# Performance work log

Measured on AMD Instinct MI355X. Metric: run time of the kernel, lower is better.

## Reference

```python
import jax, jax.numpy as jnp
import numpy as np


def _next_pow2(n: int) -> int:
    # matches torch: 2 ** ceil(log2(n))
    return 1 << (int(n) - 1).bit_length()


def setup_inputs() -> dict:
    key = jax.random.key(0)
    k1, k2 = jax.random.split(key)
    B, T, L = 256, 32768, 32768
    x = jax.random.normal(k1, (B, T), dtype=jnp.float32)
    filt = jax.random.normal(k2, (1, L), dtype=jnp.float32)
    return {"x": x, "filt": filt}


def reference(x, filt):
    """EpochedFutureFill.forward: exact causal convolution of x with filt.

    The per-token epoched algorithm (tau-step direct sum + FutureFill FFT
    cache refresh every K steps, cache initialized to zero) computes exactly
    y[b, t] = sum_{s=0}^{min(t, L-1)} filt[0, s] * x[b, t-s].
    We compute it with one FFT-based linear convolution, mirroring the
    float32 FFT math of future_fill().
    """
    B, T = x.shape
    L = filt.shape[-1]
    n_fft = _next_pow2(T + L - 1)
    xf = jnp.fft.rfft(x.astype(jnp.float32), n=n_fft)          # (B, n_fft//2+1)
    wf = jnp.fft.rfft(filt.astype(jnp.float32), n=n_fft)       # (1, n_fft//2+1)
    y = jnp.fft.irfft(xf * wf, n=n_fft)[:, :T]                 # causal lags 0..T-1
    return y.astype(x.dtype)
```

## Files before the change

kernel.cpp:

```cpp
#include <hip/hip_runtime.h>
#include <cstdint>

typedef __attribute__((ext_vector_type(8))) short short8;
typedef __attribute__((ext_vector_type(4))) float floatx4;

#define TWO_PI 6.283185307179586f

__device__ __forceinline__ unsigned short f2bf(float f) {
  union { float f; uint32_t u; } c; c.f = f;
  uint32_t u = c.u;
  u += 0x7FFFu + ((u >> 16) & 1u);
  return (unsigned short)(u >> 16);
}
__device__ __forceinline__ uint32_t packbf(float re, float im) {
  return (uint32_t)f2bf(re) | ((uint32_t)f2bf(im) << 16);
}


__global__ __launch_bounds__(256) void prep_all(
    const float* __restrict__ x, const float* __restrict__ filt,
    unsigned short* __restrict__ A1, unsigned short* __restrict__ A2,
    unsigned short* __restrict__ A3, unsigned short* __restrict__ A4,
    uint32_t* __restrict__ Zp, float2* __restrict__ Gw,
    float2* __restrict__ Tw) {
  __shared__ float2 roots[256];
  const int bid = blockIdx.x;
  const int tid = threadIdx.x;
  const float w256 = TWO_PI / 256.0f;
  if (bid < 3072) {
    int idx = bid * 256 + tid;
    if (idx < 131072) {
      int col = idx & 255, row = idx >> 8;
      int k1 = row >> 1, d = row & 1, r = col >> 1, e = col & 1;
      float th = (float)((k1 * r) & 255) * w256;
      float sn, cs; __sincosf(th, &sn, &cs);
      A1[idx] = f2bf(d == 0 ? (e == 0 ? cs : sn) : (e == 0 ? -sn : cs));
    } else if (idx < 393216) {
      int j = idx - 131072;
      int col = j & 511, row = j >> 9;
      int k2 = row >> 1, d = row & 1, cc = col >> 1, e = col & 1;
      float th = (float)((k2 * cc) & 255) * w256;
      float sn, cs; __sincosf(th, &sn, &cs);
      A2[j] = f2bf(d == 0 ? (e == 0 ? cs : sn) : (e == 0 ? -sn : cs));
    } else if (idx < 655360) {
      int j = idx - 393216;
      int col = j & 511, row = j >> 9;
      int cc = row >> 1, d = row & 1, k2 = col >> 1, e = col & 1;
      float th = (float)((k2 * cc) & 255) * w256;
      float sn, cs; __sincosf(th, &sn, &cs);
      A3[j] = f2bf(d == 0 ? (e == 0 ? cs : -sn) : (e == 0 ? sn : cs));
    } else {
      int j = idx - 655360;
      int col = j & 511, row = j >> 9;
      int r = row >> 1, d = row & 1, k1 = col >> 1, e = col & 1;
      float th = (float)((k1 * r) & 255) * w256;
      float sn, cs; __sincosf(th, &sn, &cs);
      A4[j] = f2bf(d == 0 ? (e == 0 ? cs : -sn) : (e == 0 ? sn : cs));
    }
  } else if (bid < 4096) {
    int b2 = bid - 3072;
    int s = b2 >> 3, rq = b2 & 7;
    const float* x0 = x + (size_t)(2 * s) * 32768;
    const float* x1 = x0 + 32768;
    uint32_t v[16];
    #pragma unroll
    for (int rr = 0; rr < 16; ++rr) {
      int t = tid + 256 * (rq * 16 + rr);
      v[rr] = (uint32_t)f2bf(x0[t]) | ((uint32_t)f2bf(x1[t]) << 16);
    }
    uint32_t* dst = Zp + (size_t)(s * 256 + tid) * 128 + rq * 16;
    #pragma unroll
    for (int j = 0; j < 16; j += 4)
      *(uint4*)(dst + j) = make_uint4(v[j], v[j + 1], v[j + 2], v[j + 3]);
  } else if (bid < 4352) {
    int k1 = bid - 4096, c = tid;
    { float sn, cs; __sincosf((float)tid * w256, &sn, &cs);
      roots[tid] = make_float2(cs, sn); }
    __syncthreads();
    float ar = 0.f, ai = 0.f;
    for (int r = 0; r < 128; ++r) {
      float v = filt[c + 256 * r];
      float2 wv = roots[(k1 * r) & 255];
      ar += v * wv.x; ai -= v * wv.y;
    }
    float th = (float)((k1 * c) & 65535) * (TWO_PI / 65536.0f);
    float sn, cs; __sincosf(th, &sn, &cs);
    Gw[(k1 << 8) + c] = make_float2(ar * cs + ai * sn, ai * cs - ar * sn);
  } else {
    int k1 = bid - 4352, c = tid;
    float th = (float)((k1 * c) & 65535) * (TWO_PI / 65536.0f);
    float sn, cs; __sincosf(th, &sn, &cs);
    Tw[(k1 << 8) + c] = make_float2(cs, sn);
  }
}

__global__ __launch_bounds__(256) void prep_wb(const float2* __restrict__ Gw,
                                               float2* __restrict__ WtT) {
  __shared__ float2 roots[256];
  int k1 = blockIdx.x, k2 = threadIdx.x;
  { float sn, cs; __sincosf((float)k2 * (TWO_PI / 256.0f), &sn, &cs);
    roots[k2] = make_float2(cs, sn); }
  __syncthreads();
  float ar = 0.f, ai = 0.f;
  for (int c = 0; c < 256; ++c) {
    float2 g = Gw[(k1 << 8) + c];
    float2 wv = roots[(k2 * c) & 255];
    ar += g.x * wv.x + g.y * wv.y;
    ai += g.y * wv.x - g.x * wv.y;
  }
  WtT[(k2 << 8) + k1] = make_float2(ar, ai);
}

template <int MODE, int KITERS>
__global__ __launch_bounds__(256, 2) void dft_stage(
    const unsigned short* __restrict__ Af,
    const unsigned short* __restrict__ Bd,
    uint32_t* __restrict__ outp,
    float* __restrict__ yout,
    const float2* __restrict__ tab) {
  __shared__ unsigned short Sm[32768];
  constexpr int KP = KITERS * 64;

  const int mt = blockIdx.x >> 8;
  const int nt = blockIdx.x & 255;
  const int m0 = mt * 128, n0 = nt * 128;

  const int tid = threadIdx.x;
  const int w = tid >> 6, lane = tid & 63;
  const int qlo = lane & 15, qhi = lane >> 4;
  const int wr = w >> 1, wc = w & 1;
  const int r8 = lane >> 3, pl = lane & 7, sj = pl ^ r8, q3 = qlo & 7;

  floatx4 acc[4][4];
  #pragma unroll
  for (int i = 0; i < 4; ++i)
    #pragma unroll
    for (int j = 0; j < 4; ++j) acc[i][j] = (floatx4){0.f, 0.f, 0.f, 0.f};

  auto issue = [&](int it, int buf) {
    const int k0 = it * 64;
    unsigned short* Asb = Sm + buf * 8192;
    unsigned short* Bsb = Sm + 16384 + buf * 8192;
    #pragma unroll
    for (int q = 0; q < 4; ++q) {
      const int R = w * 32 + q * 8 + r8;
      const unsigned short* gA = Af + (size_t)(m0 + R) * KP + k0 + sj * 8;
      const unsigned short* gB = Bd + (size_t)(n0 + R) * KP + k0 + sj * 8;
      __builtin_amdgcn_global_load_lds(
          (const __attribute__((address_space(1))) uint32_t*)gA,
          (__attribute__((address_space(3))) uint32_t*)&Asb[(w * 32 + q * 8) * 64], 16, 0, 0);
      __builtin_amdgcn_global_load_lds(
          (const __attribute__((address_space(1))) uint32_t*)gB,
          (__attribute__((address_space(3))) uint32_t*)&Bsb[(w * 32 + q * 8) * 64], 16, 0, 0);
    }
  };

  issue(0, 0);
  for (int it = 0; it < KITERS; ++it) {
    __syncthreads();
    if (it + 1 < KITERS) issue(it + 1, (it + 1) & 1);
    const unsigned short* Ab = Sm + (it & 1) * 8192;
    const unsigned short* Bb = Sm + 16384 + (it & 1) * 8192;
    #pragma unroll
    for (int ks = 0; ks < 2; ++ks) {
      short8 a[4], bb[4];
      #pragma unroll
      for (int im = 0; im < 4; ++im) {
        const int R = wr * 64 + im * 16 + qlo;
        a[im] = *(const short8*)&Ab[R * 64 + (((ks * 4 + qhi) ^ q3) << 3)];
      }
      #pragma unroll
      for (int in = 0; in < 4; ++in) {
        const int R = wc * 64 + in * 16 + qlo;
        bb[in] = *(const short8*)&Bb[R * 64 + (((ks * 4 + qhi) ^ q3) << 3)];
      }
      #pragma unroll
      for (int im = 0; im < 4; ++im)
        #pragma unroll
        for (int in = 0; in < 4; ++in)
          acc[im][in] = __builtin_amdgcn_mfma_f32_16x16x32_bf16(a[im], bb[in], acc[im][in], 0, 0, 0);
    }
  }

  const int s_idx = n0 >> 8;
  const int cl0 = n0 & 255;

  if (MODE == 2) {
    __syncthreads();
    uint32_t* Tr = (uint32_t*)Sm;
    #pragma unroll
    for (int im = 0; im < 4; ++im) {
      const int mloc = wr * 32 + im * 8 + qhi * 2;
      #pragma unroll
      for (int in = 0; in < 4; ++in) {
        const int nloc = wc * 64 + in * 16 + qlo;
        #pragma unroll
        for (int pp = 0; pp < 2; ++pp) {
          const int mC = (m0 >> 1) + mloc + pp;
          float re = acc[im][in][2 * pp], iv = acc[im][in][2 * pp + 1];
          float2 wv = tab[(mC << 8) + cl0 + nloc];
          float r2 = re * wv.x - iv * wv.y, i2 = re * wv.y + iv * wv.x;
          Tr[nloc * 68 + mloc + pp] = packbf(r2, i2);
        }
      }
    }
    __syncthreads();
    const int ln = tid >> 1, half = tid & 1;
    uint32_t* dst = outp + (size_t)((s_idx << 8) + cl0 + ln) * 256 + (m0 >> 1) + half * 32;
    const uint32_t* srcp = Tr + ln * 68 + half * 32;
    #pragma unroll
    for (int j = 0; j < 32; j += 4)
      *(uint4*)(dst + j) = *(const uint4*)(srcp + j);
    return;
  }

  #pragma unroll
  for (int im = 0; im < 4; ++im) {
    const int mloc = wr * 32 + im * 8 + qhi * 2;
    #pragma unroll
    for (int in = 0; in < 4; ++in) {
      const int nloc = wc * 64 + in * 16 + qlo;
      const int cloc = cl0 + nloc;
      #pragma unroll
      for (int pp = 0; pp < 2; ++pp) {
        const int mC = (m0 >> 1) + mloc + pp;
        float re = acc[im][in][2 * pp], iv = acc[im][in][2 * pp + 1];
        if (MODE == 1) {
          float2 tw = tab[(mC << 8) + cloc];
          float r2 = re * tw.x + iv * tw.y, i2 = iv * tw.x - re * tw.y;
          outp[(size_t)((s_idx << 8) + mC) * 256 + cloc] = packbf(r2, i2);
        } else if (MODE == 3) {
          float2 tw = tab[(mC << 8) + cloc];
          float r2 = re * tw.x - iv * tw.y, i2 = iv * tw.x + re * tw.y;
          outp[(size_t)((s_idx << 8) + mC) * 256 + cloc] = packbf(r2, i2);
        } else {
          const float sc = 1.0f / 65536.0f;
          float* y0 = yout + ((size_t)s_idx << 16) + (mC << 8) + cloc;
          y0[0] = re * sc;
          y0[32768] = iv * sc;
        }
      }
    }
  }
}

extern "C" void kernel_launch(void* const* d_in, const int* in_sizes, int n_in,
                              void* d_out, int out_size, void* d_ws, size_t ws_size,
                              hipStream_t stream) {
  const float* x = (const float*)d_in[0];
  const float* filt = (const float*)d_in[1];
  float* Y = (float*)d_out;

  char* ws = (char*)d_ws;
  unsigned short* A1 = (unsigned short*)(ws + 0);
  unsigned short* A2 = (unsigned short*)(ws + 0x40000);
  unsigned short* A3 = (unsigned short*)(ws + 0xC0000);
  unsigned short* A4 = (unsigned short*)(ws + 0x140000);
  float2* Gw  = (float2*)(ws + 0x180000);
  float2* WtT = (float2*)(ws + 0x200000);
  float2* Tw  = (float2*)(ws + 0x280000);
  unsigned short* Zp = (unsigned short*)(ws + (3u << 20));
  unsigned short* G2 = (unsigned short*)(ws + 19922944u);
  unsigned short* P  = (unsigned short*)(ws + 53477376u);
  unsigned short* H2 = (unsigned short*)(ws + (3u << 20));

  hipLaunchKernelGGL(prep_all, dim3(4608), dim3(256), 0, stream,
                     x, filt, A1, A2, A3, A4, (uint32_t*)Zp, Gw, Tw);
  hipLaunchKernelGGL(prep_wb, dim3(256), dim3(256), 0, stream, Gw, WtT);

  hipLaunchKernelGGL((dft_stage<1, 4>), dim3(1024), dim3(256), 0, stream,
                     A1, Zp, (uint32_t*)G2, (float*)nullptr, Tw);
  hipLaunchKernelGGL((dft_stage<2, 8>), dim3(1024), dim3(256), 0, stream,
                     A2, G2, (uint32_t*)P, (float*)nullptr, WtT);
  hipLaunchKernelGGL((dft_stage<3, 8>), dim3(1024), dim3(256), 0, stream,
                     A3, P, (uint32_t*)H2, (float*)nullptr, Tw);
  hipLaunchKernelGGL((dft_stage<4, 8>), dim3(512), dim3(256), 0, stream,
                     A4, H2, (uint32_t*)nullptr, Y, Tw);
}
```

Measured before the change: 189.5 us.

## Use 256x256 output tiles with 512-thread blocks for middle DFT stages

Adds a dft_stage_big kernel that computes a 256x256 tile per block using 8 waves (each wave 128x64) with double-buffered direct global-to-LDS loads, replacing the 128x256-tile version for stages 2 and 3. Larger tiles raise operand reuse and halve the number of blocks. The MODE 2 transposed write-back goes through an XOR-swizzled LDS buffer to avoid bank conflicts. In exchange it uses more registers and 128KB of LDS for one block per CU, so occupancy and latency hiding drop, and 256 blocks may fit the CU count poorly.

```diff
diff --git a/kernel.cpp b/kernel.cpp
--- a/kernel.cpp
+++ b/kernel.cpp
@@ -185,35 +185,6 @@
   const int s_idx = n0 >> 8;
   const int cl0 = n0 & 255;
 
-  if (MODE == 2) {
-    __syncthreads();
-    uint32_t* Tr = (uint32_t*)Sm;
-    #pragma unroll
-    for (int im = 0; im < 4; ++im) {
-      const int mloc = wr * 32 + im * 8 + qhi * 2;
-      #pragma unroll
-      for (int in = 0; in < 4; ++in) {
-        const int nloc = wc * 64 + in * 16 + qlo;
-        #pragma unroll
-        for (int pp = 0; pp < 2; ++pp) {
-          const int mC = (m0 >> 1) + mloc + pp;
-          float re = acc[im][in][2 * pp], iv = acc[im][in][2 * pp + 1];
-          float2 wv = tab[(mC << 8) + cl0 + nloc];
-          float r2 = re * wv.x - iv * wv.y, i2 = re * wv.y + iv * wv.x;
-          Tr[nloc * 68 + mloc + pp] = packbf(r2, i2);
-        }
-      }
-    }
-    __syncthreads();
-    const int ln = tid >> 1, half = tid & 1;
-    uint32_t* dst = outp + (size_t)((s_idx << 8) + cl0 + ln) * 256 + (m0 >> 1) + half * 32;
-    const uint32_t* srcp = Tr + ln * 68 + half * 32;
-    #pragma unroll
-    for (int j = 0; j < 32; j += 4)
-      *(uint4*)(dst + j) = *(const uint4*)(srcp + j);
-    return;
-  }
-
   #pragma unroll
   for (int im = 0; im < 4; ++im) {
     const int mloc = wr * 32 + im * 8 + qhi * 2;
@@ -229,16 +200,132 @@
           float2 tw = tab[(mC << 8) + cloc];
           float r2 = re * tw.x + iv * tw.y, i2 = iv * tw.x - re * tw.y;
           outp[(size_t)((s_idx << 8) + mC) * 256 + cloc] = packbf(r2, i2);
-        } else if (MODE == 3) {
-          float2 tw = tab[(mC << 8) + cloc];
-          float r2 = re * tw.x - iv * tw.y, i2 = iv * tw.x + re * tw.y;
-          outp[(size_t)((s_idx << 8) + mC) * 256 + cloc] = packbf(r2, i2);
         } else {
           const float sc = 1.0f / 65536.0f;
           float* y0 = yout + ((size_t)s_idx << 16) + (mC << 8) + cloc;
           y0[0] = re * sc;
           y0[32768] = iv * sc;
         }
+      }
+    }
+  }
+}
+
+template <int MODE, int KITERS>
+__global__ __launch_bounds__(512, 1) void dft_stage_big(
+    const unsigned short* __restrict__ Af,
+    const unsigned short* __restrict__ Bd,
+    uint32_t* __restrict__ outp,
+    const float2* __restrict__ tab) {
+  __shared__ unsigned short Sm[65536];
+  constexpr int KP = KITERS * 64;
+
+  const int mt = blockIdx.x >> 7;
+  const int s  = blockIdx.x & 127;
+  const int m0 = mt * 256, n0 = s * 256;
+
+  const int tid = threadIdx.x;
+  const int w = tid >> 6, lane = tid & 63;
+  const int qlo = lane & 15, qhi = lane >> 4;
+  const int wr = w >> 2, wc = w & 3;
+  const int r8 = lane >> 3, pl = lane & 7, sj = pl ^ r8, q3 = qlo & 7;
+
+  floatx4 acc[8][4];
+  #pragma unroll
+  for (int i = 0; i < 8; ++i)
+    #pragma unroll
+    for (int j = 0; j < 4; ++j) acc[i][j] = (floatx4){0.f, 0.f, 0.f, 0.f};
+
+  auto issue = [&](int it, int buf) {
+    const int k0 = it * 64;
+    unsigned short* Asb = Sm + buf * 16384;
+    unsigned short* Bsb = Sm + 32768 + buf * 16384;
+    #pragma unroll
+    for (int q = 0; q < 4; ++q) {
+      const int R = w * 32 + q * 8 + r8;
+      const unsigned short* gA = Af + (size_t)(m0 + R) * KP + k0 + sj * 8;
+      const unsigned short* gB = Bd + (size_t)(n0 + R) * KP + k0 + sj * 8;
+      __builtin_amdgcn_global_load_lds(
+          (const __attribute__((address_space(1))) uint32_t*)gA,
+          (__attribute__((address_space(3))) uint32_t*)&Asb[(w * 32 + q * 8) * 64], 16, 0, 0);
+      __builtin_amdgcn_global_load_lds(
+          (const __attribute__((address_space(1))) uint32_t*)gB,
+          (__attribute__((address_space(3))) uint32_t*)&Bsb[(w * 32 + q * 8) * 64], 16, 0, 0);
+    }
+  };
+
+  issue(0, 0);
+  for (int it = 0; it < KITERS; ++it) {
+    __syncthreads();
+    if (it + 1 < KITERS) issue(it + 1, (it + 1) & 1);
+    const unsigned short* Ab = Sm + (it & 1) * 16384;
+    const unsigned short* Bb = Sm + 32768 + (it & 1) * 16384;
+    #pragma unroll
+    for (int ks = 0; ks < 2; ++ks) {
+      short8 a[8], bb[4];
+      #pragma unroll
+      for (int im = 0; im < 8; ++im) {
+        const int R = wr * 128 + im * 16 + qlo;
+        a[im] = *(const short8*)&Ab[R * 64 + (((ks * 4 + qhi) ^ q3) << 3)];
+      }
+      #pragma unroll
+      for (int in = 0; in < 4; ++in) {
+        const int R = wc * 64 + in * 16 + qlo;
+        bb[in] = *(const short8*)&Bb[R * 64 + (((ks * 4 + qhi) ^ q3) << 3)];
+      }
+      #pragma unroll
+      for (int im = 0; im < 8; ++im)
+        #pragma unroll
+        for (int in = 0; in < 4; ++in)
+          acc[im][in] = __builtin_amdgcn_mfma_f32_16x16x32_bf16(a[im], bb[in], acc[im][in], 0, 0, 0);
+    }
+  }
+
+  if (MODE == 2) {
+    __syncthreads();
+    uint32_t* Tr = (uint32_t*)Sm;
+    #pragma unroll
+    for (int im = 0; im < 8; ++im) {
+      const int mbase = wr * 64 + im * 8 + qhi * 2;
+      #pragma unroll
+      for (int in = 0; in < 4; ++in) {
+        const int k1 = wc * 64 + in * 16 + qlo;
+        #pragma unroll
+        for (int pp = 0; pp < 2; ++pp) {
+          const int mlocC = mbase + pp;
+          const int k2 = mt * 128 + mlocC;
+          float re = acc[im][in][2 * pp], iv = acc[im][in][2 * pp + 1];
+          float2 wv = tab[(k2 << 8) + k1];
+          float r2 = re * wv.x - iv * wv.y, i2 = re * wv.y + iv * wv.x;
+          const int colsw = ((mlocC & 124) ^ ((k1 & 7) << 2)) + (mlocC & 3);
+          Tr[k1 * 128 + colsw] = packbf(r2, i2);
+        }
+      }
+    }
+    __syncthreads();
+    const int ln = tid >> 1, half = tid & 1;
+    uint32_t* dst = outp + (size_t)((s << 8) + ln) * 256 + mt * 128 + half * 64;
+    #pragma unroll
+    for (int j = 0; j < 64; j += 4) {
+      const int grp = (half * 64 + j) ^ ((ln & 7) << 2);
+      *(uint4*)(dst + j) = *(const uint4*)&Tr[ln * 128 + grp];
+    }
+    return;
+  }
+
+  #pragma unroll
+  for (int im = 0; im < 8; ++im) {
+    const int mbase = wr * 64 + im * 8 + qhi * 2;
+    #pragma unroll
+    for (int in = 0; in < 4; ++in) {
+      const int k1 = wc * 64 + in * 16 + qlo;
+      #pragma unroll
+      for (int pp = 0; pp < 2; ++pp) {
+        const int cC = mt * 128 + mbase + pp;
+        float re = acc[im][in][2 * pp], iv = acc[im][in][2 * pp + 1];
+        float2 tw = tab[(cC << 8) + k1];
+        float r2 = re * tw.x - iv * tw.y, i2 = iv * tw.x + re * tw.y;
+        outp[(size_t)((s << 8) + cC) * 256 + k1] = packbf(r2, i2);
       }
     }
   }
@@ -270,10 +357,10 @@
 
   hipLaunchKernelGGL((dft_stage<1, 4>), dim3(1024), dim3(256), 0, stream,
                      A1, Zp, (uint32_t*)G2, (float*)nullptr, Tw);
-  hipLaunchKernelGGL((dft_stage<2, 8>), dim3(1024), dim3(256), 0, stream,
-                     A2, G2, (uint32_t*)P, (float*)nullptr, WtT);
-  hipLaunchKernelGGL((dft_stage<3, 8>), dim3(1024), dim3(256), 0, stream,
-                     A3, P, (uint32_t*)H2, (float*)nullptr, Tw);
+  hipLaunchKernelGGL((dft_stage_big<2, 8>), dim3(256), dim3(512), 0, stream,
+                     A2, G2, (uint32_t*)P, WtT);
+  hipLaunchKernelGGL((dft_stage_big<3, 8>), dim3(256), dim3(512), 0, stream,
+                     A3, P, (uint32_t*)H2, Tw);
   hipLaunchKernelGGL((dft_stage<4, 8>), dim3(512), dim3(256), 0, stream,
                      A4, H2, (uint32_t*)nullptr, Y, Tw);
 }
```

Result: slower. 215.1 us (+13.5%).

## Fuse DFT stages 2 and 3 into one kernel keeping intermediate in LDS

Applied to the files above, without the earlier changes.

Replaces the separate stage-2 and stage-3 DFT GEMM launches with a single kernel that computes the stage-2 product, applies the spectral weight, stores the bf16 intermediate in shared memory and immediately runs the stage-3 GEMM with twiddles. This is meant to remove the global round trip of the intermediate buffer P and one launch. The trade-offs are 512-thread blocks with large LDS use (about 80KB), fewer blocks in the grid, and A-operand fragments read directly from global memory rather than staged through LDS, which may lower occupancy.

```diff
diff --git a/kernel.cpp b/kernel.cpp
--- a/kernel.cpp
+++ b/kernel.cpp
@@ -185,35 +185,6 @@
   const int s_idx = n0 >> 8;
   const int cl0 = n0 & 255;
 
-  if (MODE == 2) {
-    __syncthreads();
-    uint32_t* Tr = (uint32_t*)Sm;
-    #pragma unroll
-    for (int im = 0; im < 4; ++im) {
-      const int mloc = wr * 32 + im * 8 + qhi * 2;
-      #pragma unroll
-      for (int in = 0; in < 4; ++in) {
-        const int nloc = wc * 64 + in * 16 + qlo;
-        #pragma unroll
-        for (int pp = 0; pp < 2; ++pp) {
-          const int mC = (m0 >> 1) + mloc + pp;
-          float re = acc[im][in][2 * pp], iv = acc[im][in][2 * pp + 1];
-          float2 wv = tab[(mC << 8) + cl0 + nloc];
-          float r2 = re * wv.x - iv * wv.y, i2 = re * wv.y + iv * wv.x;
-          Tr[nloc * 68 + mloc + pp] = packbf(r2, i2);
-        }
-      }
-    }
-    __syncthreads();
-    const int ln = tid >> 1, half = tid & 1;
-    uint32_t* dst = outp + (size_t)((s_idx << 8) + cl0 + ln) * 256 + (m0 >> 1) + half * 32;
-    const uint32_t* srcp = Tr + ln * 68 + half * 32;
-    #pragma unroll
-    for (int j = 0; j < 32; j += 4)
-      *(uint4*)(dst + j) = *(const uint4*)(srcp + j);
-    return;
-  }
-
   #pragma unroll
   for (int im = 0; im < 4; ++im) {
     const int mloc = wr * 32 + im * 8 + qhi * 2;
@@ -229,16 +200,142 @@
           float2 tw = tab[(mC << 8) + cloc];
           float r2 = re * tw.x + iv * tw.y, i2 = iv * tw.x - re * tw.y;
           outp[(size_t)((s_idx << 8) + mC) * 256 + cloc] = packbf(r2, i2);
-        } else if (MODE == 3) {
-          float2 tw = tab[(mC << 8) + cloc];
-          float r2 = re * tw.x - iv * tw.y, i2 = iv * tw.x + re * tw.y;
-          outp[(size_t)((s_idx << 8) + mC) * 256 + cloc] = packbf(r2, i2);
         } else {
           const float sc = 1.0f / 65536.0f;
           float* y0 = yout + ((size_t)s_idx << 16) + (mC << 8) + cloc;
           y0[0] = re * sc;
           y0[32768] = iv * sc;
         }
+      }
+    }
+  }
+}
+
+__global__ __launch_bounds__(512) void dft_stage23(
+    const unsigned short* __restrict__ A2,
+    const unsigned short* __restrict__ A3,
+    const unsigned short* __restrict__ G2s,
+    uint32_t* __restrict__ H2u,
+    const float2* __restrict__ WtT,
+    const float2* __restrict__ Tw) {
+  __shared__ unsigned short Bst[2][4096];
+  __shared__ uint32_t Pbu[64 * 256];
+
+  const int s  = blockIdx.x >> 2;
+  const int q  = blockIdx.x & 3;
+  const int k1base = q * 64;
+
+  const int tid = threadIdx.x;
+  const int w = tid >> 6, lane = tid & 63;
+  const int qlo = lane & 15, qhi = lane >> 4;
+  const int wr = w >> 1, wc = w & 1;
+  const int srow = tid >> 3;
+  const int spl = tid & 7;
+  const int skoff = (spl ^ (srow & 7)) << 3;
+
+  floatx4 acc[8][2];
+  #pragma unroll
+  for (int i = 0; i < 8; ++i)
+    #pragma unroll
+    for (int j = 0; j < 2; ++j) acc[i][j] = (floatx4){0.f, 0.f, 0.f, 0.f};
+
+  const unsigned short* G2base = G2s + (size_t)(s * 256 + k1base) * 512;
+
+  auto issueB = [&](int kc) {
+    const unsigned short* gB = G2base + (size_t)srow * 512 + kc * 64 + skoff;
+    __builtin_amdgcn_global_load_lds(
+        (const __attribute__((address_space(1))) uint32_t*)gB,
+        (__attribute__((address_space(3))) uint32_t*)&Bst[kc & 1][w * 512], 16, 0, 0);
+  };
+
+  issueB(0);
+  for (int kc = 0; kc < 8; ++kc) {
+    __syncthreads();
+    if (kc + 1 < 8) issueB(kc + 1);
+    const unsigned short* Bb = Bst[kc & 1];
+    #pragma unroll
+    for (int ks = 0; ks < 2; ++ks) {
+      short8 a[8], bb[2];
+      #pragma unroll
+      for (int im = 0; im < 8; ++im) {
+        const int R = wr * 128 + im * 16 + qlo;
+        a[im] = *(const short8*)&A2[(size_t)R * 512 + kc * 64 + ks * 32 + qhi * 8];
+      }
+      #pragma unroll
+      for (int in = 0; in < 2; ++in) {
+        const int R = wc * 32 + in * 16 + qlo;
+        bb[in] = *(const short8*)&Bb[R * 64 + (((ks * 4 + qhi) ^ (R & 7)) << 3)];
+      }
+      #pragma unroll
+      for (int im = 0; im < 8; ++im)
+        #pragma unroll
+        for (int in = 0; in < 2; ++in)
+          acc[im][in] = __builtin_amdgcn_mfma_f32_16x16x32_bf16(a[im], bb[in], acc[im][in], 0, 0, 0);
+    }
+  }
+
+  #pragma unroll
+  for (int im = 0; im < 8; ++im) {
+    const int k2b = wr * 64 + im * 8 + qhi * 2;
+    #pragma unroll
+    for (int in = 0; in < 2; ++in) {
+      const int k1l = wc * 32 + in * 16 + qlo;
+      const int k1g = k1base + k1l;
+      #pragma unroll
+      for (int pp = 0; pp < 2; ++pp) {
+        const int k2 = k2b + pp;
+        float re = acc[im][in][2 * pp], iv = acc[im][in][2 * pp + 1];
+        float2 wv = WtT[(k2 << 8) + k1g];
+        float r2 = re * wv.x - iv * wv.y, i2 = re * wv.y + iv * wv.x;
+        const int colsw = (((k2 >> 2) ^ (k1l & 7)) << 2) | (k2 & 3);
+        Pbu[k1l * 256 + colsw] = packbf(r2, i2);
+      }
+    }
+  }
+  __syncthreads();
+
+  #pragma unroll
+  for (int i = 0; i < 8; ++i)
+    #pragma unroll
+    for (int j = 0; j < 2; ++j) acc[i][j] = (floatx4){0.f, 0.f, 0.f, 0.f};
+
+  for (int kc = 0; kc < 8; ++kc) {
+    #pragma unroll
+    for (int ks = 0; ks < 2; ++ks) {
+      short8 a[8], bb[2];
+      const int kg = kc * 8 + ks * 4 + qhi;
+      #pragma unroll
+      for (int im = 0; im < 8; ++im) {
+        const int R = wr * 128 + im * 16 + qlo;
+        a[im] = *(const short8*)&A3[(size_t)R * 512 + kc * 64 + ks * 32 + qhi * 8];
+      }
+      #pragma unroll
+      for (int in = 0; in < 2; ++in) {
+        const int R = wc * 32 + in * 16 + qlo;
+        bb[in] = *(const short8*)&Pbu[R * 256 + ((kg ^ (R & 7)) << 2)];
+      }
+      #pragma unroll
+      for (int im = 0; im < 8; ++im)
+        #pragma unroll
+        for (int in = 0; in < 2; ++in)
+          acc[im][in] = __builtin_amdgcn_mfma_f32_16x16x32_bf16(a[im], bb[in], acc[im][in], 0, 0, 0);
+    }
+  }
+
+  #pragma unroll
+  for (int im = 0; im < 8; ++im) {
+    const int cb = wr * 64 + im * 8 + qhi * 2;
+    #pragma unroll
+    for (int in = 0; in < 2; ++in) {
+      const int k1l = wc * 32 + in * 16 + qlo;
+      const int k1g = k1base + k1l;
+      #pragma unroll
+      for (int pp = 0; pp < 2; ++pp) {
+        const int c = cb + pp;
+        float re = acc[im][in][2 * pp], iv = acc[im][in][2 * pp + 1];
+        float2 tw = Tw[(c << 8) + k1g];
+        float r2 = re * tw.x - iv * tw.y, i2 = iv * tw.x + re * tw.y;
+        H2u[(size_t)((s << 8) + c) * 256 + k1g] = packbf(r2, i2);
       }
     }
   }
@@ -261,8 +358,7 @@
   float2* Tw  = (float2*)(ws + 0x280000);
   unsigned short* Zp = (unsigned short*)(ws + (3u << 20));
   unsigned short* G2 = (unsigned short*)(ws + 19922944u);
-  unsigned short* P  = (unsigned short*)(ws + 53477376u);
-  unsigned short* H2 = (unsigned short*)(ws + (3u << 20));
+  unsigned short* H2 = (unsigned short*)(ws + 53477376u);
 
   hipLaunchKernelGGL(prep_all, dim3(4608), dim3(256), 0, stream,
                      x, filt, A1, A2, A3, A4, (uint32_t*)Zp, Gw, Tw);
@@ -270,10 +366,8 @@
 
   hipLaunchKernelGGL((dft_stage<1, 4>), dim3(1024), dim3(256), 0, stream,
                      A1, Zp, (uint32_t*)G2, (float*)nullptr, Tw);
-  hipLaunchKernelGGL((dft_stage<2, 8>), dim3(1024), dim3(256), 0, stream,
-                     A2, G2, (uint32_t*)P, (float*)nullptr, WtT);
-  hipLaunchKernelGGL((dft_stage<3, 8>), dim3(1024), dim3(256), 0, stream,
-                     A3, P, (uint32_t*)H2, (float*)nullptr, Tw);
+  hipLaunchKernelGGL(dft_stage23, dim3(512), dim3(512), 0, stream,
+                     A2, A3, G2, (uint32_t*)H2, WtT, Tw);
   hipLaunchKernelGGL((dft_stage<4, 8>), dim3(512), dim3(256), 0, stream,
                      A4, H2, (uint32_t*)nullptr, Y, Tw);
 }
```

After: 285.3 us. 1.51x slower.

## Store DFT operands pre-swizzled in MFMA fragment order and load directly to registers

Applied to the files above, without the earlier changes.

Twiddle matrices and intermediate spectra are now written in a layout that matches the per-lane MFMA operand fragments, so each stage loads short8 operands straight from global memory. This removes the LDS double-buffered staging, the global_load_lds copies and their barriers. Epilogues in stages 1-3 transpose through LDS to emit the next stage's fragment layout. The cost is that operand reuse across waves now comes from cache instead of LDS, and there is no explicit prefetch pipelining.

```diff
diff --git a/kernel.cpp b/kernel.cpp
--- a/kernel.cpp
+++ b/kernel.cpp
@@ -28,30 +28,42 @@
   const int tid = threadIdx.x;
   const float w256 = TWO_PI / 256.0f;
   if (bid < 3072) {
-    int idx = bid * 256 + tid;
-    if (idx < 131072) {
-      int col = idx & 255, row = idx >> 8;
+    if (bid < 512) {
+      int j = bid * 256 + tid;
+      int jj = j & 7, ln = (j >> 3) & 63, ks = (j >> 9) & 1;
+      int t = j >> 10, M16 = t & 31, kc = t >> 5;
+      int row = M16 * 16 + (ln & 15);
+      int col = kc * 64 + ks * 32 + (ln >> 4) * 8 + jj;
       int k1 = row >> 1, d = row & 1, r = col >> 1, e = col & 1;
       float th = (float)((k1 * r) & 255) * w256;
       float sn, cs; __sincosf(th, &sn, &cs);
-      A1[idx] = f2bf(d == 0 ? (e == 0 ? cs : sn) : (e == 0 ? -sn : cs));
-    } else if (idx < 393216) {
-      int j = idx - 131072;
-      int col = j & 511, row = j >> 9;
+      A1[j] = f2bf(d == 0 ? (e == 0 ? cs : sn) : (e == 0 ? -sn : cs));
+    } else if (bid < 1536) {
+      int j = (bid - 512) * 256 + tid;
+      int jj = j & 7, ln = (j >> 3) & 63, ks = (j >> 9) & 1;
+      int t = j >> 10, M16 = t & 31, kc = t >> 5;
+      int row = M16 * 16 + (ln & 15);
+      int col = kc * 64 + ks * 32 + (ln >> 4) * 8 + jj;
       int k2 = row >> 1, d = row & 1, cc = col >> 1, e = col & 1;
       float th = (float)((k2 * cc) & 255) * w256;
       float sn, cs; __sincosf(th, &sn, &cs);
       A2[j] = f2bf(d == 0 ? (e == 0 ? cs : sn) : (e == 0 ? -sn : cs));
-    } else if (idx < 655360) {
-      int j = idx - 393216;
-      int col = j & 511, row = j >> 9;
+    } else if (bid < 2560) {
+      int j = (bid - 1536) * 256 + tid;
+      int jj = j & 7, ln = (j >> 3) & 63, ks = (j >> 9) & 1;
+      int t = j >> 10, M16 = t & 31, kc = t >> 5;
+      int row = M16 * 16 + (ln & 15);
+      int col = kc * 64 + ks * 32 + (ln >> 4) * 8 + jj;
       int cc = row >> 1, d = row & 1, k2 = col >> 1, e = col & 1;
       float th = (float)((k2 * cc) & 255) * w256;
       float sn, cs; __sincosf(th, &sn, &cs);
       A3[j] = f2bf(d == 0 ? (e == 0 ? cs : -sn) : (e == 0 ? sn : cs));
     } else {
-      int j = idx - 655360;
-      int col = j & 511, row = j >> 9;
+      int j = (bid - 2560) * 256 + tid;
+      int jj = j & 7, ln = (j >> 3) & 63, ks = (j >> 9) & 1;
+      int t = j >> 10, M16 = t & 15, kc = t >> 4;
+      int row = M16 * 16 + (ln & 15);
+      int col = kc * 64 + ks * 32 + (ln >> 4) * 8 + jj;
       int r = row >> 1, d = row & 1, k1 = col >> 1, e = col & 1;
       float th = (float)((k1 * r) & 255) * w256;
       float sn, cs; __sincosf(th, &sn, &cs);
@@ -68,10 +80,12 @@
       int t = tid + 256 * (rq * 16 + rr);
       v[rr] = (uint32_t)f2bf(x0[t]) | ((uint32_t)f2bf(x1[t]) << 16);
     }
-    uint32_t* dst = Zp + (size_t)(s * 256 + tid) * 128 + rq * 16;
-    #pragma unroll
-    for (int j = 0; j < 16; j += 4)
-      *(uint4*)(dst + j) = make_uint4(v[j], v[j + 1], v[j + 2], v[j + 3]);
+    const int kc = rq >> 1, ks = rq & 1;
+    uint32_t* dst = Zp + (size_t)s * 32768 +
+                    ((kc * 16 + (tid >> 4)) * 2 + ks) * 256 + (tid & 15) * 4;
+    #pragma unroll
+    for (int q = 0; q < 4; ++q)
+      *(uint4*)(dst + q * 64) = make_uint4(v[4*q], v[4*q+1], v[4*q+2], v[4*q+3]);
   } else if (bid < 4352) {
     int k1 = bid - 4096, c = tid;
     { float sn, cs; __sincosf((float)tid * w256, &sn, &cs);
@@ -111,25 +125,25 @@
   WtT[(k2 << 8) + k1] = make_float2(ar, ai);
 }
 
-template <int MODE, int KITERS>
-__global__ __launch_bounds__(256, 2) void dft_stage(
+template <int MODE, int KC, int MD16>
+__global__ __launch_bounds__(256, 2) void dft_stageR(
     const unsigned short* __restrict__ Af,
-    const unsigned short* __restrict__ Bd,
+    const uint32_t* __restrict__ Bf,
     uint32_t* __restrict__ outp,
     float* __restrict__ yout,
     const float2* __restrict__ tab) {
-  __shared__ unsigned short Sm[32768];
-  constexpr int KP = KITERS * 64;
+  __shared__ uint32_t Tr[(MODE == 4) ? 64 : 8704];
 
   const int mt = blockIdx.x >> 8;
   const int nt = blockIdx.x & 255;
   const int m0 = mt * 128, n0 = nt * 128;
+  const int s = n0 >> 8;
+  const int nlow = n0 & 255;
 
   const int tid = threadIdx.x;
   const int w = tid >> 6, lane = tid & 63;
   const int qlo = lane & 15, qhi = lane >> 4;
   const int wr = w >> 1, wc = w & 1;
-  const int r8 = lane >> 3, pl = lane & 7, sj = pl ^ r8, q3 = qlo & 7;
 
   floatx4 acc[4][4];
   #pragma unroll
@@ -137,105 +151,133 @@
     #pragma unroll
     for (int j = 0; j < 4; ++j) acc[i][j] = (floatx4){0.f, 0.f, 0.f, 0.f};
 
-  auto issue = [&](int it, int buf) {
-    const int k0 = it * 64;
-    unsigned short* Asb = Sm + buf * 8192;
-    unsigned short* Bsb = Sm + 16384 + buf * 8192;
-    #pragma unroll
-    for (int q = 0; q < 4; ++q) {
-      const int R = w * 32 + q * 8 + r8;
-      const unsigned short* gA = Af + (size_t)(m0 + R) * KP + k0 + sj * 8;
-      const unsigned short* gB = Bd + (size_t)(n0 + R) * KP + k0 + sj * 8;
-      __builtin_amdgcn_global_load_lds(
-          (const __attribute__((address_space(1))) uint32_t*)gA,
-          (__attribute__((address_space(3))) uint32_t*)&Asb[(w * 32 + q * 8) * 64], 16, 0, 0);
-      __builtin_amdgcn_global_load_lds(
-          (const __attribute__((address_space(1))) uint32_t*)gB,
-          (__attribute__((address_space(3))) uint32_t*)&Bsb[(w * 32 + q * 8) * 64], 16, 0, 0);
-    }
-  };
-
-  issue(0, 0);
-  for (int it = 0; it < KITERS; ++it) {
-    __syncthreads();
-    if (it + 1 < KITERS) issue(it + 1, (it + 1) & 1);
-    const unsigned short* Ab = Sm + (it & 1) * 8192;
-    const unsigned short* Bb = Sm + 16384 + (it & 1) * 8192;
+  const uint32_t* Bp = Bf + (size_t)s * (KC * 8192);
+  const int m16b = (m0 >> 4) + wr * 4;
+  const int n16b = (nlow >> 4) + wc * 4;
+
+  #pragma unroll
+  for (int kc = 0; kc < KC; ++kc) {
     #pragma unroll
     for (int ks = 0; ks < 2; ++ks) {
-      short8 a[4], bb[4];
-      #pragma unroll
-      for (int im = 0; im < 4; ++im) {
-        const int R = wr * 64 + im * 16 + qlo;
-        a[im] = *(const short8*)&Ab[R * 64 + (((ks * 4 + qhi) ^ q3) << 3)];
-      }
-      #pragma unroll
-      for (int in = 0; in < 4; ++in) {
-        const int R = wc * 64 + in * 16 + qlo;
-        bb[in] = *(const short8*)&Bb[R * 64 + (((ks * 4 + qhi) ^ q3) << 3)];
-      }
+      short8 a[4], b[4];
       #pragma unroll
       for (int im = 0; im < 4; ++im)
+        a[im] = *(const short8*)(Af +
+            (size_t)(((kc * MD16 + m16b + im) * 2 + ks) * 512 + lane * 8));
+      #pragma unroll
+      for (int in = 0; in < 4; ++in)
+        b[in] = *(const short8*)(Bp +
+            (((kc * 16 + n16b + in) * 2 + ks) * 256 + lane * 4));
+      #pragma unroll
+      for (int im = 0; im < 4; ++im)
         #pragma unroll
         for (int in = 0; in < 4; ++in)
-          acc[im][in] = __builtin_amdgcn_mfma_f32_16x16x32_bf16(a[im], bb[in], acc[im][in], 0, 0, 0);
+          acc[im][in] = __builtin_amdgcn_mfma_f32_16x16x32_bf16(
+              a[im], b[in], acc[im][in], 0, 0, 0);
     }
   }
 
-  const int s_idx = n0 >> 8;
-  const int cl0 = n0 & 255;
-
-  if (MODE == 2) {
-    __syncthreads();
-    uint32_t* Tr = (uint32_t*)Sm;
+  if constexpr (MODE == 1) {
     #pragma unroll
     for (int im = 0; im < 4; ++im) {
       const int mloc = wr * 32 + im * 8 + qhi * 2;
       #pragma unroll
       for (int in = 0; in < 4; ++in) {
         const int nloc = wc * 64 + in * 16 + qlo;
+        const int c = nlow + nloc;
+        #pragma unroll
+        for (int pp = 0; pp < 2; ++pp) {
+          const int k1loc = mloc + pp;
+          const int k1 = (m0 >> 1) + k1loc;
+          float re = acc[im][in][2*pp], iv = acc[im][in][2*pp+1];
+          float2 tw = tab[(k1 << 8) + c];
+          float r2 = re * tw.x + iv * tw.y, i2 = iv * tw.x - re * tw.y;
+          Tr[k1loc * 132 + nloc] = packbf(r2, i2);
+        }
+      }
+    }
+    __syncthreads();
+    #pragma unroll
+    for (int p = 0; p < 8; ++p) {
+      const int sb = p * 4 + w;
+      const int kcL = sb >> 3, N16l = (sb >> 1) & 3, ksb = sb & 1;
+      uint4 v = *(const uint4*)&Tr[(N16l*16 + qlo) * 132 + kcL*32 + ksb*16 + qhi*4];
+      const int kcg = (nlow >> 5) + kcL, N16g = (m0 >> 5) + N16l;
+      *(uint4*)&outp[(size_t)s * 65536 +
+                     (size_t)(((kcg * 16 + N16g) * 2 + ksb) * 256 + lane * 4)] = v;
+    }
+  } else if constexpr (MODE == 2) {
+    #pragma unroll
+    for (int im = 0; im < 4; ++im) {
+      const int mloc = wr * 32 + im * 8 + qhi * 2;
+      #pragma unroll
+      for (int in = 0; in < 4; ++in) {
+        const int nloc = wc * 64 + in * 16 + qlo;
+        const int k1 = nlow + nloc;
+        #pragma unroll
+        for (int pp = 0; pp < 2; ++pp) {
+          const int k2loc = mloc + pp;
+          const int k2 = (m0 >> 1) + k2loc;
+          float re = acc[im][in][2*pp], iv = acc[im][in][2*pp+1];
+          float2 wv = tab[(k2 << 8) + k1];
+          float r2 = re * wv.x - iv * wv.y, i2 = re * wv.y + iv * wv.x;
+          Tr[nloc * 68 + k2loc] = packbf(r2, i2);
+        }
+      }
+    }
+    __syncthreads();
+    #pragma unroll
+    for (int p = 0; p < 8; ++p) {
+      const int sb = p * 4 + w;
+      const int kcL = sb >> 4, N16l = (sb >> 1) & 7, ksb = sb & 1;
+      uint4 v = *(const uint4*)&Tr[(N16l*16 + qlo) * 68 + kcL*32 + ksb*16 + qhi*4];
+      const int kcg = (m0 >> 6) + kcL, N16g = (nlow >> 4) + N16l;
+      *(uint4*)&outp[(size_t)s * 65536 +
+                     (size_t)(((kcg * 16 + N16g) * 2 + ksb) * 256 + lane * 4)] = v;
+    }
+  } else if constexpr (MODE == 3) {
+    #pragma unroll
+    for (int im = 0; im < 4; ++im) {
+      const int mloc = wr * 32 + im * 8 + qhi * 2;
+      #pragma unroll
+      for (int in = 0; in < 4; ++in) {
+        const int nloc = wc * 64 + in * 16 + qlo;
+        const int k1 = nlow + nloc;
+        #pragma unroll
+        for (int pp = 0; pp < 2; ++pp) {
+          const int cloc = mloc + pp;
+          const int c = (m0 >> 1) + cloc;
+          float re = acc[im][in][2*pp], iv = acc[im][in][2*pp+1];
+          float2 tw = tab[(c << 8) + k1];
+          float r2 = re * tw.x - iv * tw.y, i2 = iv * tw.x + re * tw.y;
+          Tr[cloc * 132 + nloc] = packbf(r2, i2);
+        }
+      }
+    }
+    __syncthreads();
+    #pragma unroll
+    for (int p = 0; p < 8; ++p) {
+      const int sb = p * 4 + w;
+      const int kcL = sb >> 3, N16l = (sb >> 1) & 3, ksb = sb & 1;
+      uint4 v = *(const uint4*)&Tr[(N16l*16 + qlo) * 132 + kcL*32 + ksb*16 + qhi*4];
+      const int kcg = (nlow >> 5) + kcL, N16g = (m0 >> 5) + N16l;
+      *(uint4*)&outp[(size_t)s * 65536 +
+                     (size_t)(((kcg * 16 + N16g) * 2 + ksb) * 256 + lane * 4)] = v;
+    }
+  } else {
+    #pragma unroll
+    for (int im = 0; im < 4; ++im) {
+      const int mloc = wr * 32 + im * 8 + qhi * 2;
+      #pragma unroll
+      for (int in = 0; in < 4; ++in) {
+        const int nloc = wc * 64 + in * 16 + qlo;
+        const int cloc = nlow + nloc;
         #pragma unroll
         for (int pp = 0; pp < 2; ++pp) {
           const int mC = (m0 >> 1) + mloc + pp;
-          float re = acc[im][in][2 * pp], iv = acc[im][in][2 * pp + 1];
-          float2 wv = tab[(mC << 8) + cl0 + nloc];
-          float r2 = re * wv.x - iv * wv.y, i2 = re * wv.y + iv * wv.x;
-          Tr[nloc * 68 + mloc + pp] = packbf(r2, i2);
-        }
-      }
-    }
-    __syncthreads();
-    const int ln = tid >> 1, half = tid & 1;
-    uint32_t* dst = outp + (size_t)((s_idx << 8) + cl0 + ln) * 256 + (m0 >> 1) + half * 32;
-    const uint32_t* srcp = Tr + ln * 68 + half * 32;
-    #pragma unroll
-    for (int j = 0; j < 32; j += 4)
-      *(uint4*)(dst + j) = *(const uint4*)(srcp + j);
-    return;
-  }
-
-  #pragma unroll
-  for (int im = 0; im < 4; ++im) {
-    const int mloc = wr * 32 + im * 8 + qhi * 2;
-    #pragma unroll
-    for (int in = 0; in < 4; ++in) {
-      const int nloc = wc * 64 + in * 16 + qlo;
-      const int cloc = cl0 + nloc;
-      #pragma unroll
-      for (int pp = 0; pp < 2; ++pp) {
-        const int mC = (m0 >> 1) + mloc + pp;
-        float re = acc[im][in][2 * pp], iv = acc[im][in][2 * pp + 1];
-        if (MODE == 1) {
-          float2 tw = tab[(mC << 8) + cloc];
-          float r2 = re * tw.x + iv * tw.y, i2 = iv * tw.x - re * tw.y;
-          outp[(size_t)((s_idx << 8) + mC) * 256 + cloc] = packbf(r2, i2);
-        } else if (MODE == 3) {
-          float2 tw = tab[(mC << 8) + cloc];
-          float r2 = re * tw.x - iv * tw.y, i2 = iv * tw.x + re * tw.y;
-          outp[(size_t)((s_idx << 8) + mC) * 256 + cloc] = packbf(r2, i2);
-        } else {
+          float re = acc[im][in][2*pp], iv = acc[im][in][2*pp+1];
           const float sc = 1.0f / 65536.0f;
-          float* y0 = yout + ((size_t)s_idx << 16) + (mC << 8) + cloc;
+          float* y0 = yout + ((size_t)s << 16) + (mC << 8) + cloc;
           y0[0] = re * sc;
           y0[32768] = iv * sc;
         }
@@ -259,21 +301,21 @@
   float2* Gw  = (float2*)(ws + 0x180000);
   float2* WtT = (float2*)(ws + 0x200000);
   float2* Tw  = (float2*)(ws + 0x280000);
-  unsigned short* Zp = (unsigned short*)(ws + (3u << 20));
-  unsigned short* G2 = (unsigned short*)(ws + 19922944u);
-  unsigned short* P  = (unsigned short*)(ws + 53477376u);
-  unsigned short* H2 = (unsigned short*)(ws + (3u << 20));
+  uint32_t* Zp = (uint32_t*)(ws + (3u << 20));
+  uint32_t* G2 = (uint32_t*)(ws + 19922944u);
+  uint32_t* P  = (uint32_t*)(ws + 53477376u);
+  uint32_t* H2 = (uint32_t*)(ws + (3u << 20));
 
   hipLaunchKernelGGL(prep_all, dim3(4608), dim3(256), 0, stream,
-                     x, filt, A1, A2, A3, A4, (uint32_t*)Zp, Gw, Tw);
+                     x, filt, A1, A2, A3, A4, Zp, Gw, Tw);
   hipLaunchKernelGGL(prep_wb, dim3(256), dim3(256), 0, stream, Gw, WtT);
 
-  hipLaunchKernelGGL((dft_stage<1, 4>), dim3(1024), dim3(256), 0, stream,
-                     A1, Zp, (uint32_t*)G2, (float*)nullptr, Tw);
-  hipLaunchKernelGGL((dft_stage<2, 8>), dim3(1024), dim3(256), 0, stream,
-                     A2, G2, (uint32_t*)P, (float*)nullptr, WtT);
-  hipLaunchKernelGGL((dft_stage<3, 8>), dim3(1024), dim3(256), 0, stream,
-                     A3, P, (uint32_t*)H2, (float*)nullptr, Tw);
-  hipLaunchKernelGGL((dft_stage<4, 8>), dim3(512), dim3(256), 0, stream,
+  hipLaunchKernelGGL((dft_stageR<1, 4, 32>), dim3(1024), dim3(256), 0, stream,
+                     A1, Zp, G2, (float*)nullptr, Tw);
+  hipLaunchKernelGGL((dft_stageR<2, 8, 32>), dim3(1024), dim3(256), 0, stream,
+                     A2, G2, P, (float*)nullptr, WtT);
+  hipLaunchKernelGGL((dft_stageR<3, 8, 32>), dim3(1024), dim3(256), 0, stream,
+                     A3, P, H2, (float*)nullptr, Tw);
+  hipLaunchKernelGGL((dft_stageR<4, 8, 16>), dim3(512), dim3(256), 0, stream,
                      A4, H2, (uint32_t*)nullptr, Y, Tw);
 }
```

Result: slower. 197.7 us (+4.3%).
